# Performance work log

Hardware: AMD Instinct MI355X
Metric: run time of the kernel (lower is better)

## Reference

```python
import jax, jax.numpy as jnp
import numpy as np

N_NODES = 20000
N_EDGES = 320000
IN_CH = 64
OUT_CH = 128

def _gat(x, src, dst, W, a_src, a_dst, bias, concat):
    # PyG GATConv: linear -> per-edge leaky_relu attention logits -> segment softmax over dst -> scatter-weighted sum
    N = x.shape[0]
    H, C = a_src.shape
    xl = (x @ W).reshape(N, H, C)                       # [N,H,C]
    al = (xl * a_src).sum(-1)                           # [N,H] src logits
    ar = (xl * a_dst).sum(-1)                           # [N,H] dst logits
    e = jax.nn.leaky_relu(al[src] + ar[dst], 0.2)       # [E,H]
    emax = jax.ops.segment_max(e, dst, num_segments=N)  # every node has a self loop -> no empty segments
    ee = jnp.exp(e - emax[dst])
    denom = jax.ops.segment_sum(ee, dst, num_segments=N)
    alpha = ee / (denom[dst] + 1e-16)                   # [E,H]
    out = jax.ops.segment_sum(xl[src] * alpha[:, :, None], dst, num_segments=N)  # [N,H,C]
    out = out.reshape(N, H * C) if concat else out.mean(axis=1)
    return out + bias

def setup_inputs() -> dict:
    key = jax.random.key(0)
    ks = jax.random.split(key, 32)
    def lin(k, fi, fo):
        return jax.random.normal(k, (fi, fo), jnp.float32) / np.sqrt(fi)
    def att(k, H, C):
        return jax.random.normal(k, (H, C), jnp.float32) / np.sqrt(C)
    x = jax.random.normal(ks[0], (N_NODES, IN_CH), jnp.float32)
    src = jax.random.randint(ks[1], (N_EDGES,), 0, N_NODES, jnp.int32)
    dst = jax.random.randint(ks[2], (N_EDGES,), 0, N_NODES, jnp.int32)
    dst = jnp.where(dst == src, (dst + 1) % N_NODES, dst)  # avoid pre-existing self loops
    edge_index = jnp.stack([src, dst])
    edge_time = jax.random.uniform(ks[3], (N_EDGES,), jnp.float32)
    H = 4
    return {
        "x": x, "edge_time": edge_time,
        "W1": lin(ks[4], IN_CH, 512), "as1": att(ks[5], H, 128), "ad1": att(ks[6], H, 128), "b1": jnp.zeros((512,), jnp.float32),
        "W2": lin(ks[7], 512, 512),   "as2": att(ks[8], H, 128), "ad2": att(ks[9], H, 128), "b2": jnp.zeros((512,), jnp.float32),
        "W3": lin(ks[10], 512, 512),  "as3": att(ks[11], H, 128), "ad3": att(ks[12], H, 128), "b3": jnp.zeros((OUT_CH,), jnp.float32),
        "tW1": lin(ks[13], 1, 64), "tb1": jnp.zeros((64,), jnp.float32),
        "tW2": lin(ks[14], 64, OUT_CH), "tb2": jnp.zeros((OUT_CH,), jnp.float32),
        "fW1": lin(ks[15], 2 * OUT_CH, OUT_CH), "fb1": jnp.zeros((OUT_CH,), jnp.float32),
        "fW2": lin(ks[16], OUT_CH, OUT_CH), "fb2": jnp.zeros((OUT_CH,), jnp.float32),
        "ln_g": jnp.ones((OUT_CH,), jnp.float32), "ln_b": jnp.zeros((OUT_CH,), jnp.float32),
        "rW": lin(ks[17], IN_CH, OUT_CH), "rb": jnp.zeros((OUT_CH,), jnp.float32),
        "edge_index": edge_index,
    }

def reference(x, edge_time, W1, as1, ad1, b1, W2, as2, ad2, b2, W3, as3, ad3, b3,
              tW1, tb1, tW2, tb2, fW1, fb1, fW2, fb2, ln_g, ln_b, rW, rb, edge_index):
    N = x.shape[0]
    loop = jnp.arange(N, dtype=edge_index.dtype)
    src = jnp.concatenate([edge_index[0], loop])
    dst = jnp.concatenate([edge_index[1], loop])
    # temporal embedding of raw (pre-self-loop) edges
    t = edge_time[:, None]
    time_emb = jax.nn.relu(t @ tW1 + tb1) @ tW2 + tb2    # [E, OUT_CH]
    x_res = x @ rW + rb
    h = jax.nn.relu(_gat(x, src, dst, W1, as1, ad1, b1, True))
    h = jax.nn.relu(_gat(h, src, dst, W2, as2, ad2, b2, True))
    h = jax.nn.relu(_gat(h, src, dst, W3, as3, ad3, b3, False))
    # x_agg[row] += h[col]  with (row, col) = (src, dst) incl. self loops
    agg = jax.ops.segment_sum(h[dst], src, num_segments=N)
    tm = jnp.broadcast_to(time_emb.mean(axis=0)[None, :], (N, time_emb.shape[1]))
    z = jnp.concatenate([agg, tm], axis=1)
    z = jax.nn.relu(z @ fW1 + fb1)                        # dropout is identity in eval
    z = z @ fW2 + fb2
    mu = z.mean(-1, keepdims=True)
    var = ((z - mu) ** 2).mean(-1, keepdims=True)
    z = (z - mu) / jnp.sqrt(var + 1e-5) * ln_g + ln_b
    return z + x_res
```

## Files before the change

### kernel.cpp

```cpp
#include <hip/hip_runtime.h>
#include <hip/hip_bf16.h>
#include <math.h>

typedef short bf16x8 __attribute__((ext_vector_type(8)));
typedef float f32x4 __attribute__((ext_vector_type(4)));

__device__ __forceinline__ float lrelu(float v) { return v > 0.f ? v : 0.2f * v; }

__device__ __forceinline__ void gload16(const void* g, void* l) {
  __builtin_amdgcn_global_load_lds(
      (const __attribute__((address_space(1))) void*)g,
      (__attribute__((address_space(3))) void*)l, 16, 0, 0);
}

__device__ __forceinline__ uint packbf(float v0, float v1) {
  __hip_bfloat16 h0 = __float2bfloat16(v0);
  __hip_bfloat16 h1 = __float2bfloat16(v1);
  return (uint)(*(unsigned short*)&h0) | ((uint)(*(unsigned short*)&h1) << 16);
}

__global__ __launch_bounds__(256) void k_countT(const int* __restrict__ src,
    const int* __restrict__ dst, int E, int* cntD, int* cntS,
    const float* __restrict__ et, const float* __restrict__ tW1,
    const float* __restrict__ tb1, float* __restrict__ tacc) {
  int t = threadIdx.x;
  int e = blockIdx.x * 256 + t;
  if (e < E) {
    atomicAdd(&cntD[dst[e]], 1);
    atomicAdd(&cntS[src[e]], 1);
  }
  if (blockIdx.x < 256) {
    __shared__ float se[256];
    __shared__ float buf[256];
    int l = t & 63, w = t >> 6;
    float wk = tW1[l], bk = tb1[l];
    float a0 = 0.f, a1 = 0.f, a2 = 0.f, a3 = 0.f;
    for (int base = blockIdx.x * 256; base < E; base += 256 * 256) {
      int idx = base + t;
      se[t] = (idx < E) ? et[idx] : 0.f;
      __syncthreads();
      int cnt = E - base; if (cnt > 256) cnt = 256;
      int s0 = w * 64;
      int c = cnt - s0; if (c < 0) c = 0; if (c > 64) c = 64;
      int j = 0;
      for (; j + 4 <= c; j += 4) {
        a0 += fmaxf(se[s0 + j] * wk + bk, 0.f);
        a1 += fmaxf(se[s0 + j + 1] * wk + bk, 0.f);
        a2 += fmaxf(se[s0 + j + 2] * wk + bk, 0.f);
        a3 += fmaxf(se[s0 + j + 3] * wk + bk, 0.f);
      }
      for (; j < c; ++j) a0 += fmaxf(se[s0 + j] * wk + bk, 0.f);
      __syncthreads();
    }
    buf[t] = (a0 + a1) + (a2 + a3);
    __syncthreads();
    if (t < 64) {
      float s = buf[t] + buf[t + 64] + buf[t + 128] + buf[t + 192];
      atomicAdd(&tacc[t], s);
    }
  }
}

__global__ __launch_bounds__(1024) void k_scan2c(const int* __restrict__ cntD, int* __restrict__ offD,
    const int* __restrict__ cntS, int* __restrict__ offS, int n,
    const float* __restrict__ tacc, const float* __restrict__ tW2,
    const float* __restrict__ tb2, const float* __restrict__ fW1,
    const float* __restrict__ fb1, float* __restrict__ cvec, int E) {
  int t = threadIdx.x;
  if (blockIdx.x == 2) {
    __shared__ float tm[128];
    if (t < 128) {
      float inv = 1.f / (float)E;
      float acc = tb2[t];
      for (int k = 0; k < 64; ++k) acc += (tacc[k] * inv) * tW2[k * 128 + t];
      tm[t] = acc;
    }
    __syncthreads();
    if (t < 128) {
      float c = fb1[t];
      for (int k = 0; k < 128; ++k) c += tm[k] * fW1[(128 + k) * 128 + t];
      cvec[t] = c;
    }
    return;
  }
  const int* cnt = blockIdx.x ? cntS : cntD;
  int* off = blockIdx.x ? offS : offD;
  __shared__ int sums[1024];
  int PT = (n + 1023) >> 10;
  int start = t * PT;
  int local = 0;
  for (int i = 0; i < PT; ++i) {
    int idx = start + i;
    if (idx < n) local += cnt[idx];
  }
  sums[t] = local;
  __syncthreads();
  for (int o = 1; o < 1024; o <<= 1) {
    int v = (t >= o) ? sums[t - o] : 0;
    __syncthreads();
    sums[t] += v;
    __syncthreads();
  }
  int run = sums[t] - local;
  for (int i = 0; i < PT; ++i) {
    int idx = start + i;
    if (idx < n) { off[idx] = run; run += cnt[idx]; }
  }
  if (t == 1023) off[n] = run;
}

__global__ void k_fill(const int* __restrict__ src, const int* __restrict__ dst, int E,
                       const int* __restrict__ offD, int* curD, int* lstD,
                       const int* __restrict__ offS, int* curS, int* lstS) {
  int e = blockIdx.x * blockDim.x + threadIdx.x;
  if (e < E) {
    int d = dst[e], s = src[e];
    int p = atomicAdd(&curD[d], 1);
    lstD[offD[d] + p] = s;
    int q = atomicAdd(&curS[s], 1);
    lstS[offS[s] + q] = d;
  }
}

struct PrepArgs {
  const float* W[6]; __hip_bfloat16* Wt[6]; int K[6]; int Nw[6]; int tstart[6];
  int NC, XB;
};

__global__ __launch_bounds__(256) void k_prep(PrepArgs a, const float* __restrict__ x,
    __hip_bfloat16* __restrict__ xbf, __hip_bfloat16* __restrict__ habf,
    __hip_bfloat16* __restrict__ aggbf, int N, int Mp) {
  __shared__ float tile[32][65];
  int bid = blockIdx.x;
  int t = threadIdx.x;
  if (bid < a.NC) {
    int m = 0;
#pragma unroll
    for (int i = 1; i < 6; ++i) if (bid >= a.tstart[i]) m = i;
    const float* W = a.W[m];
    __hip_bfloat16* Wt = a.Wt[m];
    int K = a.K[m], Nw = a.Nw[m];
    int lt = bid - a.tstart[m];
    int ntn = Nw >> 6;
    int bk = (lt / ntn) * 32, bn = (lt % ntn) * 64;
    int rn = t & 63, rk = t >> 6;
#pragma unroll
    for (int i = 0; i < 8; ++i)
      tile[rk + i * 4][rn] = W[(size_t)(bk + rk + i * 4) * Nw + bn + rn];
    __syncthreads();
    int wk2 = (t & 15) * 2, wn = t >> 4;
    uint* Wo = (uint*)Wt;
#pragma unroll
    for (int i = 0; i < 4; ++i) {
      int n = wn + i * 16;
      Wo[((size_t)(bn + n) * K + bk + wk2) >> 1] = packbf(tile[wk2][n], tile[wk2 + 1][n]);
    }
  } else if (bid < a.NC + a.XB) {
    int i4 = (bid - a.NC) * 256 + t;
    int row = i4 >> 4;
    float4 v = make_float4(0.f, 0.f, 0.f, 0.f);
    if (row < N) v = ((const float4*)x)[i4];
    uint2 p; p.x = packbf(v.x, v.y); p.y = packbf(v.z, v.w);
    ((uint2*)xbf)[i4] = p;
  } else {
    int row = N + (bid - a.NC - a.XB);
    ((uint*)habf)[(size_t)row * 256 + t] = 0;
    if (t < 64) ((uint*)aggbf)[(size_t)row * 64 + t] = 0;
  }
}

template<int EPI>
__global__ __launch_bounds__(256) void gemm_t(
    const __hip_bfloat16* __restrict__ A, const __hip_bfloat16* __restrict__ Bt,
    void* __restrict__ Cout, const float* __restrict__ bias,
    int M, int Nw, int K, int relu, int Nn,
    const float* __restrict__ asrc, const float* __restrict__ adst,
    float* __restrict__ al, float* __restrict__ ar,
    float* __restrict__ C2, const float* __restrict__ bias2,
    const float* __restrict__ lng, const float* __restrict__ lnb,
    float* __restrict__ resid)
{
  __shared__ short As0[128 * 32];
  __shared__ short As1[128 * 32];
  __shared__ short Bs0[128 * 32];
  __shared__ short Bs1[128 * 32];
  int tid = threadIdx.x;
  int bm = blockIdx.x * 128;
  int cb = blockIdx.y;
  int bn = cb * 128;
  int w = tid >> 6, l = tid & 63;
  int wr = (w >> 1) * 64, wc = (w & 1) * 64;
  f32x4 acc[4][4] = {};
  const short* Ag = (const short*)A;
  const short* Bg = (const short*)Bt;

  for (int k0 = 0; k0 < K; k0 += 64) {
#pragma unroll
    for (int i = 0; i < 2; ++i) {
      int slot = i * 256 + tid;
      int row = slot >> 2;
      int col = (slot & 3) * 8;
      const short* Arow = Ag + (size_t)(bm + row) * K + k0 + col;
      const short* Brow = Bg + (size_t)(bn + row) * K + k0 + col;
      gload16(Arow, &As0[slot * 8]);
      gload16(Arow + 32, &As1[slot * 8]);
      gload16(Brow, &Bs0[slot * 8]);
      gload16(Brow + 32, &Bs1[slot * 8]);
    }
    __syncthreads();
    {
      bf16x8 af[4], bfr[4];
#pragma unroll
      for (int m = 0; m < 4; ++m)
        af[m] = *(const bf16x8*)&As0[(wr + m * 16 + (l & 15)) * 32 + (l >> 4) * 8];
#pragma unroll
      for (int n = 0; n < 4; ++n)
        bfr[n] = *(const bf16x8*)&Bs0[(wc + n * 16 + (l & 15)) * 32 + (l >> 4) * 8];
#pragma unroll
      for (int m = 0; m < 4; ++m)
#pragma unroll
        for (int n = 0; n < 4; ++n)
          acc[m][n] = __builtin_amdgcn_mfma_f32_16x16x32_bf16(af[m], bfr[n], acc[m][n], 0, 0, 0);
    }
    {
      bf16x8 af[4], bfr[4];
#pragma unroll
      for (int m = 0; m < 4; ++m)
        af[m] = *(const bf16x8*)&As1[(wr + m * 16 + (l & 15)) * 32 + (l >> 4) * 8];
#pragma unroll
      for (int n = 0; n < 4; ++n)
        bfr[n] = *(const bf16x8*)&Bs1[(wc + n * 16 + (l & 15)) * 32 + (l >> 4) * 8];
#pragma unroll
      for (int m = 0; m < 4; ++m)
#pragma unroll
        for (int n = 0; n < 4; ++n)
          acc[m][n] = __builtin_amdgcn_mfma_f32_16x16x32_bf16(af[m], bfr[n], acc[m][n], 0, 0, 0);
    }
    __syncthreads();
  }

  int g = l >> 4, cc = l & 15, cr = g * 4;

  if (EPI == 0) {
#pragma unroll
    for (int n = 0; n < 4; ++n) {
      int col = bn + wc + n * 16 + cc;
      float bb = bias ? bias[col] : 0.f;
#pragma unroll
      for (int m = 0; m < 4; ++m) {
#pragma unroll
        for (int r = 0; r < 4; ++r) {
          int gm = bm + wr + m * 16 + cr + r;
          if (gm < M) {
            float v = acc[m][n][r] + bb;
            if (relu) v = fmaxf(v, 0.f);
            ((__hip_bfloat16*)Cout)[(size_t)gm * Nw + col] = __float2bfloat16(v);
          }
        }
      }
    }
  }

  if (EPI == 1) {
    if (cb < 4) {
#pragma unroll
      for (int n = 0; n < 4; ++n) {
        int col = bn + wc + n * 16 + cc;
#pragma unroll
        for (int m = 0; m < 4; ++m) {
#pragma unroll
          for (int r = 0; r < 4; ++r) {
            int gm = bm + wr + m * 16 + cr + r;
            if (gm < M)
              ((__hip_bfloat16*)Cout)[(size_t)gm * 512 + col] = __float2bfloat16(acc[m][n][r]);
          }
        }
      }
      float asv[4], adv[4];
#pragma unroll
      for (int n = 0; n < 4; ++n) {
        int ch = bn + wc + n * 16 + cc;
        asv[n] = asrc[ch]; adv[n] = adst[ch];
      }
      float* spal = (float*)As0;
      float* spar = spal + 256;
#pragma unroll
      for (int m = 0; m < 4; ++m) {
#pragma unroll
        for (int r = 0; r < 4; ++r) {
          float pa = acc[m][0][r] * asv[0] + acc[m][1][r] * asv[1]
                   + acc[m][2][r] * asv[2] + acc[m][3][r] * asv[3];
          float pb = acc[m][0][r] * adv[0] + acc[m][1][r] * adv[1]
                   + acc[m][2][r] * adv[2] + acc[m][3][r] * adv[3];
#pragma unroll
          for (int o = 1; o < 16; o <<= 1) {
            pa += __shfl_xor(pa, o);
            pb += __shfl_xor(pb, o);
          }
          if (cc == 0) {
            int rl = m * 16 + cr + r;
            spal[w * 64 + rl] = pa;
            spar[w * 64 + rl] = pb;
          }
        }
      }
      __syncthreads();
      if ((w & 1) == 0) {
        float av = spal[w * 64 + l] + spal[(w + 1) * 64 + l];
        float rv = spar[w * 64 + l] + spar[(w + 1) * 64 + l];
        int row = bm + wr + l;
        if (row < Nn) { al[row * 4 + cb] = av; ar[row * 4 + cb] = rv; }
      }
    } else {
#pragma unroll
      for (int n = 0; n < 4; ++n) {
        int col2 = wc + n * 16 + cc;
        float bb = bias2[col2];
#pragma unroll
        for (int m = 0; m < 4; ++m) {
#pragma unroll
          for (int r = 0; r < 4; ++r) {
            int gm = bm + wr + m * 16 + cr + r;
            if (gm < Nn) C2[(size_t)gm * 128 + col2] = acc[m][n][r] + bb;
          }
        }
      }
    }
  }

  if (EPI == 2) {
    float bb[4], gl_[4], gb_[4];
#pragma unroll
    for (int n = 0; n < 4; ++n) {
      int col = wc + n * 16 + cc;
      bb[n] = bias[col]; gl_[n] = lng[col]; gb_[n] = lnb[col];
    }
    float* ssum = (float*)As0;
    float* ssq = ssum + 256;
    float* smu = ssum + 512;
    float* srs = ssum + 640;
#pragma unroll
    for (int m = 0; m < 4; ++m) {
#pragma unroll
      for (int r = 0; r < 4; ++r) {
        float s = 0.f, q = 0.f;
#pragma unroll
        for (int n = 0; n < 4; ++n) {
          float z = acc[m][n][r] + bb[n];
          s += z; q += z * z;
        }
#pragma unroll
        for (int o = 1; o < 16; o <<= 1) {
          s += __shfl_xor(s, o);
          q += __shfl_xor(q, o);
        }
        if (cc == 0) {
          int rl = m * 16 + cr + r;
          ssum[w * 64 + rl] = s;
          ssq[w * 64 + rl] = q;
        }
      }
    }
    __syncthreads();
    if ((w & 1) == 0) {
      float s = ssum[w * 64 + l] + ssum[(w + 1) * 64 + l];
      float q = ssq[w * 64 + l] + ssq[(w + 1) * 64 + l];
      float mu = s * (1.f / 128.f);
      float var = q * (1.f / 128.f) - mu * mu;
      smu[wr + l] = mu;
      srs[wr + l] = rsqrtf(var + 1e-5f);
    }
    __syncthreads();
#pragma unroll
    for (int m = 0; m < 4; ++m) {
#pragma unroll
      for (int r = 0; r < 4; ++r) {
        int rl = wr + m * 16 + cr + r;
        int gm = bm + rl;
        if (gm < M) {
          float mu = smu[rl], rs = srs[rl];
#pragma unroll
          for (int n = 0; n < 4; ++n) {
            int col = wc + n * 16 + cc;
            float z = acc[m][n][r] + bb[n];
            float y = (z - mu) * rs * gl_[n] + gb_[n] + resid[(size_t)gm * 128 + col];
            resid[(size_t)gm * 128 + col] = y;
          }
        }
      }
    }
  }
}

__global__ __launch_bounds__(256) void k_gat_agg(
    const __hip_bfloat16* __restrict__ xl, const float* __restrict__ al,
    const float* __restrict__ ar, const int* __restrict__ off,
    const int* __restrict__ lst, const float* __restrict__ bias,
    __hip_bfloat16* __restrict__ outb, __hip_bfloat16* __restrict__ outh,
    int mode, int N)
{
  __shared__ int   sside[4][64];
  __shared__ float sebuf[4][4][68];
  int w = threadIdx.x >> 6, l = threadIdx.x & 63;
  int d = blockIdx.x * 4 + w;
  bool active = (d < N);
  int base = 0, deg = 0, tot = 0;
  float4 arv = make_float4(0.f, 0.f, 0.f, 0.f);
  if (active) {
    base = off[d]; deg = off[d + 1] - base; tot = deg + 1;
    arv = *(const float4*)(ar + 4 * d);
  }
  int hh = l >> 4;
  float facc[8] = {0.f, 0.f, 0.f, 0.f, 0.f, 0.f, 0.f, 0.f};
  float dn0 = 0.f, dn1 = 0.f, dn2 = 0.f, dn3 = 0.f;
  const uint4* xw = (const uint4*)xl;
  auto fma8 = [&](uint4 pv, float e) {
    facc[0] += e * __uint_as_float(pv.x << 16);
    facc[1] += e * __uint_as_float(pv.x & 0xffff0000u);
    facc[2] += e * __uint_as_float(pv.y << 16);
    facc[3] += e * __uint_as_float(pv.y & 0xffff0000u);
    facc[4] += e * __uint_as_float(pv.z << 16);
    facc[5] += e * __uint_as_float(pv.z & 0xffff0000u);
    facc[6] += e * __uint_as_float(pv.w << 16);
    facc[7] += e * __uint_as_float(pv.w & 0xffff0000u);
  };
  for (int cb = 0; cb < tot; cb += 64) {
    int j = cb + l;
    float e0 = 0.f, e1 = 0.f, e2 = 0.f, e3 = 0.f;
    int sid = 0;
    if (j < tot) {
      sid = (j == deg) ? d : lst[base + j];
      float4 av = *(const float4*)(al + 4 * sid);
      e0 = __expf(lrelu(av.x + arv.x));
      e1 = __expf(lrelu(av.y + arv.y));
      e2 = __expf(lrelu(av.z + arv.z));
      e3 = __expf(lrelu(av.w + arv.w));
      dn0 += e0; dn1 += e1; dn2 += e2; dn3 += e3;
    }
    sside[w][l] = sid;
    sebuf[w][0][l] = e0; sebuf[w][1][l] = e1;
    sebuf[w][2][l] = e2; sebuf[w][3][l] = e3;
    int cnt = tot - cb; if (cnt > 64) cnt = 64;
    int jj = 0;
    for (; jj + 4 <= cnt; jj += 4) {
      int s0 = sside[w][jj], s1 = sside[w][jj + 1];
      int s2 = sside[w][jj + 2], s3 = sside[w][jj + 3];
      float ea = sebuf[w][hh][jj], eb = sebuf[w][hh][jj + 1];
      float ec = sebuf[w][hh][jj + 2], ed = sebuf[w][hh][jj + 3];
      uint4 p0 = xw[(size_t)s0 * 64 + l];
      uint4 p1 = xw[(size_t)s1 * 64 + l];
      uint4 p2 = xw[(size_t)s2 * 64 + l];
      uint4 p3 = xw[(size_t)s3 * 64 + l];
      fma8(p0, ea); fma8(p1, eb); fma8(p2, ec); fma8(p3, ed);
    }
    for (; jj < cnt; ++jj) {
      int s0 = sside[w][jj];
      float ea = sebuf[w][hh][jj];
      uint4 p0 = xw[(size_t)s0 * 64 + l];
      fma8(p0, ea);
    }
  }
#pragma unroll
  for (int o = 1; o < 64; o <<= 1) {
    dn0 += __shfl_xor(dn0, o); dn1 += __shfl_xor(dn1, o);
    dn2 += __shfl_xor(dn2, o); dn3 += __shfl_xor(dn3, o);
  }
  if (!active) return;
  float dsel = hh == 0 ? dn0 : hh == 1 ? dn1 : hh == 2 ? dn2 : dn3;
  float rden = 1.f / dsel;
  if (mode == 0) {
    int c8 = l * 8;
    const float4* bp = (const float4*)(bias + c8);
    float4 b0 = bp[0], b1 = bp[1];
    float vb[8] = {b0.x, b0.y, b0.z, b0.w, b1.x, b1.y, b1.z, b1.w};
    uint4 o4; uint* po = (uint*)&o4;
#pragma unroll
    for (int i = 0; i < 4; ++i) {
      float v0 = fmaxf(facc[2*i]   * rden + vb[2*i],   0.f);
      float v1 = fmaxf(facc[2*i+1] * rden + vb[2*i+1], 0.f);
      po[i] = packbf(v0, v1);
    }
    ((uint4*)outb)[(size_t)d * 64 + l] = o4;
  } else {
#pragma unroll
    for (int i = 0; i < 8; ++i) {
      facc[i] *= rden;
      facc[i] += __shfl_xor(facc[i], 16);
      facc[i] += __shfl_xor(facc[i], 32);
    }
    if (l < 16) {
      int c = l * 8;
      const float4* bp = (const float4*)(bias + c);
      float4 b0 = bp[0], b1 = bp[1];
      float vb[8] = {b0.x, b0.y, b0.z, b0.w, b1.x, b1.y, b1.z, b1.w};
      uint4 o4; uint* po = (uint*)&o4;
#pragma unroll
      for (int i = 0; i < 4; ++i) {
        float v0 = fmaxf(facc[2*i]   * 0.25f + vb[2*i],   0.f);
        float v1 = fmaxf(facc[2*i+1] * 0.25f + vb[2*i+1], 0.f);
        po[i] = packbf(v0, v1);
      }
      ((uint4*)outh)[(size_t)d * 16 + l] = o4;
    }
  }
}

__global__ __launch_bounds__(256) void k_aggsrc(const __hip_bfloat16* __restrict__ h3,
    const int* __restrict__ off, const int* __restrict__ lst,
    __hip_bfloat16* __restrict__ out, int N) {
  int w = threadIdx.x >> 6, l = threadIdx.x & 63;
  int n = blockIdx.x * 4 + w;
  if (n >= N) return;
  const uint* hw = (const uint*)h3;
  uint pv = hw[(size_t)n * 64 + l];
  float a0 = __uint_as_float(pv << 16);
  float a1 = __uint_as_float(pv & 0xffff0000u);
  float b0 = 0.f, b1 = 0.f, c0 = 0.f, c1 = 0.f, d0 = 0.f, d1 = 0.f;
  int b = off[n], e = off[n + 1];
  int j = b;
  for (; j + 4 <= e; j += 4) {
    int s0 = lst[j], s1 = lst[j + 1], s2 = lst[j + 2], s3 = lst[j + 3];
    uint q0 = hw[(size_t)s0 * 64 + l];
    uint q1 = hw[(size_t)s1 * 64 + l];
    uint q2 = hw[(size_t)s2 * 64 + l];
    uint q3 = hw[(size_t)s3 * 64 + l];
    a0 += __uint_as_float(q0 << 16); a1 += __uint_as_float(q0 & 0xffff0000u);
    b0 += __uint_as_float(q1 << 16); b1 += __uint_as_float(q1 & 0xffff0000u);
    c0 += __uint_as_float(q2 << 16); c1 += __uint_as_float(q2 & 0xffff0000u);
    d0 += __uint_as_float(q3 << 16); d1 += __uint_as_float(q3 & 0xffff0000u);
  }
  for (; j < e; ++j) {
    uint q = hw[(size_t)lst[j] * 64 + l];
    a0 += __uint_as_float(q << 16);
    a1 += __uint_as_float(q & 0xffff0000u);
  }
  ((uint*)out)[(size_t)n * 64 + l] = packbf((a0 + b0) + (c0 + d0), (a1 + b1) + (c1 + d1));
}

extern "C" void kernel_launch(void* const* d_in, const int* in_sizes, int n_in,
                              void* d_out, int out_size, void* d_ws, size_t ws_size,
                              hipStream_t stream) {
  (void)n_in; (void)out_size; (void)ws_size;
  const float* x   = (const float*)d_in[0];
  const float* et  = (const float*)d_in[1];
  const float* W1  = (const float*)d_in[2];
  const float* as1 = (const float*)d_in[3];
  const float* ad1 = (const float*)d_in[4];
  const float* b1  = (const float*)d_in[5];
  const float* W2  = (const float*)d_in[6];
  const float* as2 = (const float*)d_in[7];
  const float* ad2 = (const float*)d_in[8];
  const float* b2  = (const float*)d_in[9];
  const float* W3  = (const float*)d_in[10];
  const float* as3 = (const float*)d_in[11];
  const float* ad3 = (const float*)d_in[12];
  const float* b3  = (const float*)d_in[13];
  const float* tW1 = (const float*)d_in[14];
  const float* tb1 = (const float*)d_in[15];
  const float* tW2 = (const float*)d_in[16];
  const float* tb2 = (const float*)d_in[17];
  const float* fW1 = (const float*)d_in[18];
  const float* fb1 = (const float*)d_in[19];
  const float* fW2 = (const float*)d_in[20];
  const float* fb2 = (const float*)d_in[21];
  const float* lng = (const float*)d_in[22];
  const float* lnb = (const float*)d_in[23];
  const float* rW  = (const float*)d_in[24];
  const float* rb  = (const float*)d_in[25];
  const int*   ei  = (const int*)d_in[26];
  const int N = in_sizes[0] / 64;
  const int E = in_sizes[26] / 2;
  const int Mp = ((N + 127) / 128) * 128;
  const int* src = ei;
  const int* dst = ei + E;

  char* cur = (char*)d_ws;
  auto carve = [&](size_t bytes) { char* p = cur; cur += (bytes + 255) & ~(size_t)255; return p; };
  __hip_bfloat16* xbf  = (__hip_bfloat16*)carve((size_t)Mp * 64 * 2);
  __hip_bfloat16* habf = (__hip_bfloat16*)carve((size_t)Mp * 512 * 2);
  __hip_bfloat16* xlbf = (__hip_bfloat16*)carve((size_t)Mp * 512 * 2);
  __hip_bfloat16* wtCat= (__hip_bfloat16*)carve((size_t)640 * 64 * 2);
  __hip_bfloat16* wt2  = (__hip_bfloat16*)carve((size_t)512 * 512 * 2);
  __hip_bfloat16* wt3  = (__hip_bfloat16*)carve((size_t)512 * 512 * 2);
  __hip_bfloat16* wtF1 = (__hip_bfloat16*)carve((size_t)128 * 128 * 2);
  __hip_bfloat16* wtF2 = (__hip_bfloat16*)carve((size_t)128 * 128 * 2);
  __hip_bfloat16* aggbf= (__hip_bfloat16*)carve((size_t)Mp * 128 * 2);
  __hip_bfloat16* z1bf = (__hip_bfloat16*)carve((size_t)Mp * 128 * 2);
  __hip_bfloat16* h3   = (__hip_bfloat16*)carve((size_t)N * 128 * 2);
  float* al   = (float*)carve((size_t)N * 4 * 4);
  float* ar   = (float*)carve((size_t)N * 4 * 4);
  float* cvec = (float*)carve(128 * 4);
  int* offD = (int*)carve((size_t)(N + 1) * 4);
  int* offS = (int*)carve((size_t)(N + 1) * 4);
  int* lstD = (int*)carve((size_t)E * 4);
  int* lstS = (int*)carve((size_t)E * 4);
  char* zstart = cur;
  int* cntD = (int*)carve((size_t)N * 4);
  int* curD = (int*)carve((size_t)N * 4);
  int* cntS = (int*)carve((size_t)N * 4);
  int* curS = (int*)carve((size_t)N * 4);
  float* tacc = (float*)carve(64 * 4);
  size_t zbytes = (size_t)(cur - zstart);
  float* xres = (float*)d_out;

  hipMemsetAsync(zstart, 0, zbytes, stream);

  k_countT<<<(E + 255) / 256, 256, 0, stream>>>(src, dst, E, cntD, cntS, et, tW1, tb1, tacc);
  k_scan2c<<<3, 1024, 0, stream>>>(cntD, offD, cntS, offS, N, tacc, tW2, tb2, fW1, fb1, cvec, E);
  k_fill<<<(E + 255) / 256, 256, 0, stream>>>(src, dst, E, offD, curD, lstD, offS, curS, lstS);

  {
    PrepArgs pa;
    int ts = 0;
    auto setd = [&](int i, const float* W, __hip_bfloat16* Wt, int K, int Nw) {
      pa.W[i] = W; pa.Wt[i] = Wt; pa.K[i] = K; pa.Nw[i] = Nw; pa.tstart[i] = ts;
      ts += (K / 32) * (Nw / 64);
    };
    setd(0, W1, wtCat, 64, 512);
    setd(1, W2, wt2, 512, 512);
    setd(2, W3, wt3, 512, 512);
    setd(3, rW, wtCat + (size_t)512 * 64, 64, 128);
    setd(4, fW1, wtF1, 128, 128);
    setd(5, fW2, wtF2, 128, 128);
    pa.NC = ts;
    pa.XB = Mp / 16;
    int grid = pa.NC + pa.XB + (Mp - N);
    k_prep<<<grid, 256, 0, stream>>>(pa, x, xbf, habf, aggbf, N, Mp);
  }

  const int TB = Mp / 128;
  const int GB = (N + 3) / 4;

  gemm_t<1><<<dim3(TB, 5), 256, 0, stream>>>(xbf, wtCat, xlbf, nullptr, Mp, 640, 64, 0, N,
      as1, ad1, al, ar, xres, rb, nullptr, nullptr, nullptr);
  k_gat_agg<<<GB, 256, 0, stream>>>(xlbf, al, ar, offD, lstD, b1, habf, nullptr, 0, N);
  gemm_t<1><<<dim3(TB, 4), 256, 0, stream>>>(habf, wt2, xlbf, nullptr, Mp, 512, 512, 0, N,
      as2, ad2, al, ar, nullptr, nullptr, nullptr, nullptr, nullptr);
  k_gat_agg<<<GB, 256, 0, stream>>>(xlbf, al, ar, offD, lstD, b2, habf, nullptr, 0, N);
  gemm_t<1><<<dim3(TB, 4), 256, 0, stream>>>(habf, wt3, xlbf, nullptr, Mp, 512, 512, 0, N,
      as3, ad3, al, ar, nullptr, nullptr, nullptr, nullptr, nullptr);
  k_gat_agg<<<GB, 256, 0, stream>>>(xlbf, al, ar, offD, lstD, b3, nullptr, h3, 1, N);

  k_aggsrc<<<GB, 256, 0, stream>>>(h3, offS, lstS, aggbf, N);

  gemm_t<0><<<dim3(TB, 1), 256, 0, stream>>>(aggbf, wtF1, z1bf, cvec, Mp, 128, 128, 1, N,
      nullptr, nullptr, nullptr, nullptr, nullptr, nullptr, nullptr, nullptr, nullptr);
  gemm_t<2><<<dim3(TB, 1), 256, 0, stream>>>(z1bf, wtF2, nullptr, fb2, N, 128, 128, 0, N,
      nullptr, nullptr, nullptr, nullptr, nullptr, nullptr, lng, lnb, xres);
}
```

Baseline: 380.4 us.

## Merge setup kernels, fold CSR fill into first GEMM, fuse FFN GEMMs

Merges the edge-count/time-embedding kernel with the weight-conversion prep kernel into a single launch. Folds the CSR fill pass into extra blocks of the first GEMM grid, so it runs alongside that GEMM. Fuses the two feed-forward GEMMs into one kernel that keeps the intermediate in LDS, removing the z1 round trip through global memory. This cuts launch count and global traffic, at the cost of larger LDS use in the fused FFN kernel and heterogeneous block roles.

```diff
diff --git a/kernel.cpp b/kernel.cpp
--- a/kernel.cpp
+++ b/kernel.cpp
@@ -19,45 +19,94 @@
   return (uint)(*(unsigned short*)&h0) | ((uint)(*(unsigned short*)&h1) << 16);
 }
 
-__global__ __launch_bounds__(256) void k_countT(const int* __restrict__ src,
-    const int* __restrict__ dst, int E, int* cntD, int* cntS,
+struct PrepArgs {
+  const float* W[6]; __hip_bfloat16* Wt[6]; int K[6]; int Nw[6]; int tstart[6];
+  int NC, XB;
+};
+
+__global__ __launch_bounds__(256) void k_build(
+    const int* __restrict__ src, const int* __restrict__ dst, int E,
+    int* cntD, int* cntS,
     const float* __restrict__ et, const float* __restrict__ tW1,
-    const float* __restrict__ tb1, float* __restrict__ tacc) {
+    const float* __restrict__ tb1, float* __restrict__ tacc,
+    PrepArgs a, const float* __restrict__ x,
+    __hip_bfloat16* __restrict__ xbf, __hip_bfloat16* __restrict__ habf,
+    __hip_bfloat16* __restrict__ aggbf, int N, int Mp, int EB) {
+  __shared__ float se[256];
+  __shared__ float buf[256];
+  __shared__ float tile[32][65];
   int t = threadIdx.x;
-  int e = blockIdx.x * 256 + t;
-  if (e < E) {
-    atomicAdd(&cntD[dst[e]], 1);
-    atomicAdd(&cntS[src[e]], 1);
-  }
-  if (blockIdx.x < 256) {
-    __shared__ float se[256];
-    __shared__ float buf[256];
-    int l = t & 63, w = t >> 6;
-    float wk = tW1[l], bk = tb1[l];
-    float a0 = 0.f, a1 = 0.f, a2 = 0.f, a3 = 0.f;
-    for (int base = blockIdx.x * 256; base < E; base += 256 * 256) {
-      int idx = base + t;
-      se[t] = (idx < E) ? et[idx] : 0.f;
+  int bid = blockIdx.x;
+  if (bid < EB) {
+    int e = bid * 256 + t;
+    if (e < E) {
+      atomicAdd(&cntD[dst[e]], 1);
+      atomicAdd(&cntS[src[e]], 1);
+    }
+    if (bid < 256) {
+      int l = t & 63, w = t >> 6;
+      float wk = tW1[l], bk = tb1[l];
+      float a0 = 0.f, a1 = 0.f, a2 = 0.f, a3 = 0.f;
+      for (int base = bid * 256; base < E; base += 256 * 256) {
+        int idx = base + t;
+        se[t] = (idx < E) ? et[idx] : 0.f;
+        __syncthreads();
+        int cnt = E - base; if (cnt > 256) cnt = 256;
+        int s0 = w * 64;
+        int c = cnt - s0; if (c < 0) c = 0; if (c > 64) c = 64;
+        int j = 0;
+        for (; j + 4 <= c; j += 4) {
+          a0 += fmaxf(se[s0 + j] * wk + bk, 0.f);
+          a1 += fmaxf(se[s0 + j + 1] * wk + bk, 0.f);
+          a2 += fmaxf(se[s0 + j + 2] * wk + bk, 0.f);
+          a3 += fmaxf(se[s0 + j + 3] * wk + bk, 0.f);
+        }
+        for (; j < c; ++j) a0 += fmaxf(se[s0 + j] * wk + bk, 0.f);
+        __syncthreads();
+      }
+      buf[t] = (a0 + a1) + (a2 + a3);
       __syncthreads();
-      int cnt = E - base; if (cnt > 256) cnt = 256;
-      int s0 = w * 64;
-      int c = cnt - s0; if (c < 0) c = 0; if (c > 64) c = 64;
-      int j = 0;
-      for (; j + 4 <= c; j += 4) {
-        a0 += fmaxf(se[s0 + j] * wk + bk, 0.f);
-        a1 += fmaxf(se[s0 + j + 1] * wk + bk, 0.f);
-        a2 += fmaxf(se[s0 + j + 2] * wk + bk, 0.f);
-        a3 += fmaxf(se[s0 + j + 3] * wk + bk, 0.f);
-      }
-      for (; j < c; ++j) a0 += fmaxf(se[s0 + j] * wk + bk, 0.f);
-      __syncthreads();
-    }
-    buf[t] = (a0 + a1) + (a2 + a3);
-    __syncthreads();
-    if (t < 64) {
-      float s = buf[t] + buf[t + 64] + buf[t + 128] + buf[t + 192];
-      atomicAdd(&tacc[t], s);
-    }
+      if (t < 64) {
+        float s = buf[t] + buf[t + 64] + buf[t + 128] + buf[t + 192];
+        atomicAdd(&tacc[t], s);
+      }
+    }
+    return;
+  }
+  int pbid = bid - EB;
+  if (pbid < a.NC) {
+    int m = 0;
+#pragma unroll
+    for (int i = 1; i < 6; ++i) if (pbid >= a.tstart[i]) m = i;
+    const float* W = a.W[m];
+    __hip_bfloat16* Wt = a.Wt[m];
+    int K = a.K[m], Nw = a.Nw[m];
+    int lt = pbid - a.tstart[m];
+    int ntn = Nw >> 6;
+    int bk = (lt / ntn) * 32, bn = (lt % ntn) * 64;
+    int rn = t & 63, rk = t >> 6;
+#pragma unroll
+    for (int i = 0; i < 8; ++i)
+      tile[rk + i * 4][rn] = W[(size_t)(bk + rk + i * 4) * Nw + bn + rn];
+    __syncthreads();
+    int wk2 = (t & 15) * 2, wn = t >> 4;
+    uint* Wo = (uint*)Wt;
+#pragma unroll
+    for (int i = 0; i < 4; ++i) {
+      int n = wn + i * 16;
+      Wo[((size_t)(bn + n) * K + bk + wk2) >> 1] = packbf(tile[wk2][n], tile[wk2 + 1][n]);
+    }
+  } else if (pbid < a.NC + a.XB) {
+    int i4 = (pbid - a.NC) * 256 + t;
+    int row = i4 >> 4;
+    float4 v = make_float4(0.f, 0.f, 0.f, 0.f);
+    if (row < N) v = ((const float4*)x)[i4];
+    uint2 p; p.x = packbf(v.x, v.y); p.y = packbf(v.z, v.w);
+    ((uint2*)xbf)[i4] = p;
+  } else {
+    int row = N + (pbid - a.NC - a.XB);
+    ((uint*)habf)[(size_t)row * 256 + t] = 0;
+    if (t < 64) ((uint*)aggbf)[(size_t)row * 64 + t] = 0;
   }
 }
 
@@ -109,81 +158,34 @@
   if (t == 1023) off[n] = run;
 }
 
-__global__ void k_fill(const int* __restrict__ src, const int* __restrict__ dst, int E,
-                       const int* __restrict__ offD, int* curD, int* lstD,
-                       const int* __restrict__ offS, int* curS, int* lstS) {
-  int e = blockIdx.x * blockDim.x + threadIdx.x;
-  if (e < E) {
-    int d = dst[e], s = src[e];
-    int p = atomicAdd(&curD[d], 1);
-    lstD[offD[d] + p] = s;
-    int q = atomicAdd(&curS[s], 1);
-    lstS[offS[s] + q] = d;
-  }
-}
-
-struct PrepArgs {
-  const float* W[6]; __hip_bfloat16* Wt[6]; int K[6]; int Nw[6]; int tstart[6];
-  int NC, XB;
-};
-
-__global__ __launch_bounds__(256) void k_prep(PrepArgs a, const float* __restrict__ x,
-    __hip_bfloat16* __restrict__ xbf, __hip_bfloat16* __restrict__ habf,
-    __hip_bfloat16* __restrict__ aggbf, int N, int Mp) {
-  __shared__ float tile[32][65];
-  int bid = blockIdx.x;
-  int t = threadIdx.x;
-  if (bid < a.NC) {
-    int m = 0;
-#pragma unroll
-    for (int i = 1; i < 6; ++i) if (bid >= a.tstart[i]) m = i;
-    const float* W = a.W[m];
-    __hip_bfloat16* Wt = a.Wt[m];
-    int K = a.K[m], Nw = a.Nw[m];
-    int lt = bid - a.tstart[m];
-    int ntn = Nw >> 6;
-    int bk = (lt / ntn) * 32, bn = (lt % ntn) * 64;
-    int rn = t & 63, rk = t >> 6;
-#pragma unroll
-    for (int i = 0; i < 8; ++i)
-      tile[rk + i * 4][rn] = W[(size_t)(bk + rk + i * 4) * Nw + bn + rn];
-    __syncthreads();
-    int wk2 = (t & 15) * 2, wn = t >> 4;
-    uint* Wo = (uint*)Wt;
-#pragma unroll
-    for (int i = 0; i < 4; ++i) {
-      int n = wn + i * 16;
-      Wo[((size_t)(bn + n) * K + bk + wk2) >> 1] = packbf(tile[wk2][n], tile[wk2 + 1][n]);
-    }
-  } else if (bid < a.NC + a.XB) {
-    int i4 = (bid - a.NC) * 256 + t;
-    int row = i4 >> 4;
-    float4 v = make_float4(0.f, 0.f, 0.f, 0.f);
-    if (row < N) v = ((const float4*)x)[i4];
-    uint2 p; p.x = packbf(v.x, v.y); p.y = packbf(v.z, v.w);
-    ((uint2*)xbf)[i4] = p;
-  } else {
-    int row = N + (bid - a.NC - a.XB);
-    ((uint*)habf)[(size_t)row * 256 + t] = 0;
-    if (t < 64) ((uint*)aggbf)[(size_t)row * 64 + t] = 0;
-  }
-}
-
-template<int EPI>
-__global__ __launch_bounds__(256) void gemm_t(
+__global__ __launch_bounds__(256) void gemm_e1(
     const __hip_bfloat16* __restrict__ A, const __hip_bfloat16* __restrict__ Bt,
-    void* __restrict__ Cout, const float* __restrict__ bias,
-    int M, int Nw, int K, int relu, int Nn,
+    void* __restrict__ Cout, int M, int Nn, int K,
     const float* __restrict__ asrc, const float* __restrict__ adst,
     float* __restrict__ al, float* __restrict__ ar,
     float* __restrict__ C2, const float* __restrict__ bias2,
-    const float* __restrict__ lng, const float* __restrict__ lnb,
-    float* __restrict__ resid)
+    int TBx,
+    const int* __restrict__ fsrc, const int* __restrict__ fdst, int fE,
+    const int* __restrict__ foffD, int* fcurD, int* flstD,
+    const int* __restrict__ foffS, int* fcurS, int* flstS)
 {
   __shared__ short As0[128 * 32];
   __shared__ short As1[128 * 32];
   __shared__ short Bs0[128 * 32];
   __shared__ short Bs1[128 * 32];
+  if ((int)blockIdx.x >= TBx) {
+    if (blockIdx.y == 0) {
+      int e = ((int)blockIdx.x - TBx) * 256 + (int)threadIdx.x;
+      if (e < fE) {
+        int d = fdst[e], s = fsrc[e];
+        int p = atomicAdd(&fcurD[d], 1);
+        flstD[foffD[d] + p] = s;
+        int q = atomicAdd(&fcurS[s], 1);
+        flstS[foffS[s] + q] = d;
+      }
+    }
+    return;
+  }
   int tid = threadIdx.x;
   int bm = blockIdx.x * 128;
   int cb = blockIdx.y;
@@ -241,151 +243,259 @@
 
   int g = l >> 4, cc = l & 15, cr = g * 4;
 
-  if (EPI == 0) {
+  if (cb < 4) {
 #pragma unroll
     for (int n = 0; n < 4; ++n) {
       int col = bn + wc + n * 16 + cc;
-      float bb = bias ? bias[col] : 0.f;
 #pragma unroll
       for (int m = 0; m < 4; ++m) {
 #pragma unroll
         for (int r = 0; r < 4; ++r) {
           int gm = bm + wr + m * 16 + cr + r;
-          if (gm < M) {
-            float v = acc[m][n][r] + bb;
-            if (relu) v = fmaxf(v, 0.f);
-            ((__hip_bfloat16*)Cout)[(size_t)gm * Nw + col] = __float2bfloat16(v);
-          }
+          if (gm < M)
+            ((__hip_bfloat16*)Cout)[(size_t)gm * 512 + col] = __float2bfloat16(acc[m][n][r]);
         }
       }
     }
-  }
-
-  if (EPI == 1) {
-    if (cb < 4) {
-#pragma unroll
-      for (int n = 0; n < 4; ++n) {
-        int col = bn + wc + n * 16 + cc;
-#pragma unroll
-        for (int m = 0; m < 4; ++m) {
-#pragma unroll
-          for (int r = 0; r < 4; ++r) {
-            int gm = bm + wr + m * 16 + cr + r;
-            if (gm < M)
-              ((__hip_bfloat16*)Cout)[(size_t)gm * 512 + col] = __float2bfloat16(acc[m][n][r]);
-          }
-        }
-      }
-      float asv[4], adv[4];
-#pragma unroll
-      for (int n = 0; n < 4; ++n) {
-        int ch = bn + wc + n * 16 + cc;
-        asv[n] = asrc[ch]; adv[n] = adst[ch];
-      }
-      float* spal = (float*)As0;
-      float* spar = spal + 256;
-#pragma unroll
-      for (int m = 0; m < 4; ++m) {
-#pragma unroll
-        for (int r = 0; r < 4; ++r) {
-          float pa = acc[m][0][r] * asv[0] + acc[m][1][r] * asv[1]
-                   + acc[m][2][r] * asv[2] + acc[m][3][r] * asv[3];
-          float pb = acc[m][0][r] * adv[0] + acc[m][1][r] * adv[1]
-                   + acc[m][2][r] * adv[2] + acc[m][3][r] * adv[3];
-#pragma unroll
-          for (int o = 1; o < 16; o <<= 1) {
-            pa += __shfl_xor(pa, o);
-            pb += __shfl_xor(pb, o);
-          }
-          if (cc == 0) {
-            int rl = m * 16 + cr + r;
-            spal[w * 64 + rl] = pa;
-            spar[w * 64 + rl] = pb;
-          }
-        }
-      }
-      __syncthreads();
-      if ((w & 1) == 0) {
-        float av = spal[w * 64 + l] + spal[(w + 1) * 64 + l];
-        float rv = spar[w * 64 + l] + spar[(w + 1) * 64 + l];
-        int row = bm + wr + l;
-        if (row < Nn) { al[row * 4 + cb] = av; ar[row * 4 + cb] = rv; }
-      }
-    } else {
-#pragma unroll
-      for (int n = 0; n < 4; ++n) {
-        int col2 = wc + n * 16 + cc;
-        float bb = bias2[col2];
-#pragma unroll
-        for (int m = 0; m < 4; ++m) {
-#pragma unroll
-          for (int r = 0; r < 4; ++r) {
-            int gm = bm + wr + m * 16 + cr + r;
-            if (gm < Nn) C2[(size_t)gm * 128 + col2] = acc[m][n][r] + bb;
-          }
-        }
-      }
-    }
-  }
-
-  if (EPI == 2) {
-    float bb[4], gl_[4], gb_[4];
+    float asv[4], adv[4];
 #pragma unroll
     for (int n = 0; n < 4; ++n) {
-      int col = wc + n * 16 + cc;
-      bb[n] = bias[col]; gl_[n] = lng[col]; gb_[n] = lnb[col];
-    }
-    float* ssum = (float*)As0;
-    float* ssq = ssum + 256;
-    float* smu = ssum + 512;
-    float* srs = ssum + 640;
+      int ch = bn + wc + n * 16 + cc;
+      asv[n] = asrc[ch]; adv[n] = adst[ch];
+    }
+    float* spal = (float*)As0;
+    float* spar = spal + 256;
 #pragma unroll
     for (int m = 0; m < 4; ++m) {
 #pragma unroll
       for (int r = 0; r < 4; ++r) {
-        float s = 0.f, q = 0.f;
-#pragma unroll
-        for (int n = 0; n < 4; ++n) {
-          float z = acc[m][n][r] + bb[n];
-          s += z; q += z * z;
-        }
+        float pa = acc[m][0][r] * asv[0] + acc[m][1][r] * asv[1]
+                 + acc[m][2][r] * asv[2] + acc[m][3][r] * asv[3];
+        float pb = acc[m][0][r] * adv[0] + acc[m][1][r] * adv[1]
+                 + acc[m][2][r] * adv[2] + acc[m][3][r] * adv[3];
 #pragma unroll
         for (int o = 1; o < 16; o <<= 1) {
-          s += __shfl_xor(s, o);
-          q += __shfl_xor(q, o);
+          pa += __shfl_xor(pa, o);
+          pb += __shfl_xor(pb, o);
         }
         if (cc == 0) {
           int rl = m * 16 + cr + r;
-          ssum[w * 64 + rl] = s;
-          ssq[w * 64 + rl] = q;
+          spal[w * 64 + rl] = pa;
+          spar[w * 64 + rl] = pb;
         }
       }
     }
     __syncthreads();
     if ((w & 1) == 0) {
-      float s = ssum[w * 64 + l] + ssum[(w + 1) * 64 + l];
-      float q = ssq[w * 64 + l] + ssq[(w + 1) * 64 + l];
-      float mu = s * (1.f / 128.f);
-      float var = q * (1.f / 128.f) - mu * mu;
-      smu[wr + l] = mu;
-      srs[wr + l] = rsqrtf(var + 1e-5f);
-    }
-    __syncthreads();
+      float av = spal[w * 64 + l] + spal[(w + 1) * 64 + l];
+      float rv = spar[w * 64 + l] + spar[(w + 1) * 64 + l];
+      int row = bm + wr + l;
+      if (row < Nn) { al[row * 4 + cb] = av; ar[row * 4 + cb] = rv; }
+    }
+  } else {
+#pragma unroll
+    for (int n = 0; n < 4; ++n) {
+      int col2 = wc + n * 16 + cc;
+      float bb = bias2[col2];
+#pragma unroll
+      for (int m = 0; m < 4; ++m) {
+#pragma unroll
+        for (int r = 0; r < 4; ++r) {
+          int gm = bm + wr + m * 16 + cr + r;
+          if (gm < Nn) C2[(size_t)gm * 128 + col2] = acc[m][n][r] + bb;
+        }
+      }
+    }
+  }
+}
+
+__global__ __launch_bounds__(256) void gemm_ff(
+    const __hip_bfloat16* __restrict__ A, const __hip_bfloat16* __restrict__ B1t,
+    const __hip_bfloat16* __restrict__ B2t, const float* __restrict__ cvec,
+    const float* __restrict__ fb2, const float* __restrict__ lng,
+    const float* __restrict__ lnb, float* __restrict__ resid, int M)
+{
+  __shared__ char ldsraw[32768 + 128 * 136 * 2];
+  short* As0 = (short*)ldsraw;
+  short* As1 = As0 + 4096;
+  short* Bs0 = As1 + 4096;
+  short* Bs1 = Bs0 + 4096;
+  short* z1s = (short*)(ldsraw + 32768);
+  int tid = threadIdx.x;
+  int bm = blockIdx.x * 128;
+  int w = tid >> 6, l = tid & 63;
+  int wr = (w >> 1) * 64, wc = (w & 1) * 64;
+  int g = l >> 4, cc = l & 15, cr = g * 4;
+  const short* Ag = (const short*)A;
+  const short* B1 = (const short*)B1t;
+  const short* B2 = (const short*)B2t;
+  f32x4 acc[4][4] = {};
+
+  for (int k0 = 0; k0 < 128; k0 += 64) {
+#pragma unroll
+    for (int i = 0; i < 2; ++i) {
+      int slot = i * 256 + tid;
+      int row = slot >> 2;
+      int col = (slot & 3) * 8;
+      const short* Arow = Ag + (size_t)(bm + row) * 128 + k0 + col;
+      const short* Brow = B1 + (size_t)row * 128 + k0 + col;
+      gload16(Arow, &As0[slot * 8]);
+      gload16(Arow + 32, &As1[slot * 8]);
+      gload16(Brow, &Bs0[slot * 8]);
+      gload16(Brow + 32, &Bs1[slot * 8]);
+    }
+    __syncthreads();
+    {
+      bf16x8 af[4], bfr[4];
+#pragma unroll
+      for (int m = 0; m < 4; ++m)
+        af[m] = *(const bf16x8*)&As0[(wr + m * 16 + (l & 15)) * 32 + (l >> 4) * 8];
+#pragma unroll
+      for (int n = 0; n < 4; ++n)
+        bfr[n] = *(const bf16x8*)&Bs0[(wc + n * 16 + (l & 15)) * 32 + (l >> 4) * 8];
+#pragma unroll
+      for (int m = 0; m < 4; ++m)
+#pragma unroll
+        for (int n = 0; n < 4; ++n)
+          acc[m][n] = __builtin_amdgcn_mfma_f32_16x16x32_bf16(af[m], bfr[n], acc[m][n], 0, 0, 0);
+    }
+    {
+      bf16x8 af[4], bfr[4];
+#pragma unroll
+      for (int m = 0; m < 4; ++m)
+        af[m] = *(const bf16x8*)&As1[(wr + m * 16 + (l & 15)) * 32 + (l >> 4) * 8];
+#pragma unroll
+      for (int n = 0; n < 4; ++n)
+        bfr[n] = *(const bf16x8*)&Bs1[(wc + n * 16 + (l & 15)) * 32 + (l >> 4) * 8];
+#pragma unroll
+      for (int m = 0; m < 4; ++m)
+#pragma unroll
+        for (int n = 0; n < 4; ++n)
+          acc[m][n] = __builtin_amdgcn_mfma_f32_16x16x32_bf16(af[m], bfr[n], acc[m][n], 0, 0, 0);
+    }
+    __syncthreads();
+  }
+
+#pragma unroll
+  for (int n = 0; n < 4; ++n) {
+    int col = wc + n * 16 + cc;
+    float bb = cvec[col];
 #pragma unroll
     for (int m = 0; m < 4; ++m) {
 #pragma unroll
       for (int r = 0; r < 4; ++r) {
         int rl = wr + m * 16 + cr + r;
-        int gm = bm + rl;
-        if (gm < M) {
-          float mu = smu[rl], rs = srs[rl];
-#pragma unroll
-          for (int n = 0; n < 4; ++n) {
-            int col = wc + n * 16 + cc;
-            float z = acc[m][n][r] + bb[n];
-            float y = (z - mu) * rs * gl_[n] + gb_[n] + resid[(size_t)gm * 128 + col];
-            resid[(size_t)gm * 128 + col] = y;
-          }
+        float v = fmaxf(acc[m][n][r] + bb, 0.f);
+        __hip_bfloat16 hb = __float2bfloat16(v);
+        z1s[rl * 136 + col] = *(short*)&hb;
+      }
+    }
+  }
+#pragma unroll
+  for (int m = 0; m < 4; ++m)
+#pragma unroll
+    for (int n = 0; n < 4; ++n)
+      acc[m][n] = (f32x4){0.f, 0.f, 0.f, 0.f};
+  __syncthreads();
+
+  for (int k0 = 0; k0 < 128; k0 += 64) {
+#pragma unroll
+    for (int i = 0; i < 2; ++i) {
+      int slot = i * 256 + tid;
+      int row = slot >> 2;
+      int col = (slot & 3) * 8;
+      const short* Brow = B2 + (size_t)row * 128 + k0 + col;
+      gload16(Brow, &Bs0[slot * 8]);
+      gload16(Brow + 32, &Bs1[slot * 8]);
+    }
+    __syncthreads();
+    {
+      bf16x8 af[4], bfr[4];
+#pragma unroll
+      for (int m = 0; m < 4; ++m)
+        af[m] = *(const bf16x8*)&z1s[(wr + m * 16 + (l & 15)) * 136 + k0 + (l >> 4) * 8];
+#pragma unroll
+      for (int n = 0; n < 4; ++n)
+        bfr[n] = *(const bf16x8*)&Bs0[(wc + n * 16 + (l & 15)) * 32 + (l >> 4) * 8];
+#pragma unroll
+      for (int m = 0; m < 4; ++m)
+#pragma unroll
+        for (int n = 0; n < 4; ++n)
+          acc[m][n] = __builtin_amdgcn_mfma_f32_16x16x32_bf16(af[m], bfr[n], acc[m][n], 0, 0, 0);
+    }
+    {
+      bf16x8 af[4], bfr[4];
+#pragma unroll
+      for (int m = 0; m < 4; ++m)
+        af[m] = *(const bf16x8*)&z1s[(wr + m * 16 + (l & 15)) * 136 + k0 + 32 + (l >> 4) * 8];
+#pragma unroll
+      for (int n = 0; n < 4; ++n)
+        bfr[n] = *(const bf16x8*)&Bs1[(wc + n * 16 + (l & 15)) * 32 + (l >> 4) * 8];
+#pragma unroll
+      for (int m = 0; m < 4; ++m)
+#pragma unroll
+        for (int n = 0; n < 4; ++n)
+          acc[m][n] = __builtin_amdgcn_mfma_f32_16x16x32_bf16(af[m], bfr[n], acc[m][n], 0, 0, 0);
+    }
+    __syncthreads();
+  }
+
+  float bb[4], gl_[4], gb_[4];
+#pragma unroll
+  for (int n = 0; n < 4; ++n) {
+    int col = wc + n * 16 + cc;
+    bb[n] = fb2[col]; gl_[n] = lng[col]; gb_[n] = lnb[col];
+  }
+  float* ssum = (float*)As0;
+  float* ssq = ssum + 256;
+  float* smu = ssum + 512;
+  float* srs = ssum + 640;
+#pragma unroll
+  for (int m = 0; m < 4; ++m) {
+#pragma unroll
+    for (int r = 0; r < 4; ++r) {
+      float s = 0.f, q = 0.f;
+#pragma unroll
+      for (int n = 0; n < 4; ++n) {
+        float z = acc[m][n][r] + bb[n];
+        s += z; q += z * z;
+      }
+#pragma unroll
+      for (int o = 1; o < 16; o <<= 1) {
+        s += __shfl_xor(s, o);
+        q += __shfl_xor(q, o);
+      }
+      if (cc == 0) {
+        int rl = m * 16 + cr + r;
+        ssum[w * 64 + rl] = s;
+        ssq[w * 64 + rl] = q;
+      }
+    }
+  }
+  __syncthreads();
+  if ((w & 1) == 0) {
+    float s = ssum[w * 64 + l] + ssum[(w + 1) * 64 + l];
+    float q = ssq[w * 64 + l] + ssq[(w + 1) * 64 + l];
+    float mu = s * (1.f / 128.f);
+    float var = q * (1.f / 128.f) - mu * mu;
+    smu[wr + l] = mu;
+    srs[wr + l] = rsqrtf(var + 1e-5f);
+  }
+  __syncthreads();
+#pragma unroll
+  for (int m = 0; m < 4; ++m) {
+#pragma unroll
+    for (int r = 0; r < 4; ++r) {
+      int rl = wr + m * 16 + cr + r;
+      int gm = bm + rl;
+      if (gm < M) {
+        float mu = smu[rl], rs = srs[rl];
+#pragma unroll
+        for (int n = 0; n < 4; ++n) {
+          int col = wc + n * 16 + cc;
+          float z = acc[m][n][r] + bb[n];
+          float y = (z - mu) * rs * gl_[n] + gb_[n] + resid[(size_t)gm * 128 + col];
+          resid[(size_t)gm * 128 + col] = y;
         }
       }
     }
@@ -585,7 +695,6 @@
   __hip_bfloat16* wtF1 = (__hip_bfloat16*)carve((size_t)128 * 128 * 2);
   __hip_bfloat16* wtF2 = (__hip_bfloat16*)carve((size_t)128 * 128 * 2);
   __hip_bfloat16* aggbf= (__hip_bfloat16*)carve((size_t)Mp * 128 * 2);
-  __hip_bfloat16* z1bf = (__hip_bfloat16*)carve((size_t)Mp * 128 * 2);
   __hip_bfloat16* h3   = (__hip_bfloat16*)carve((size_t)N * 128 * 2);
   float* al   = (float*)carve((size_t)N * 4 * 4);
   float* ar   = (float*)carve((size_t)N * 4 * 4);
@@ -605,12 +714,9 @@
 
   hipMemsetAsync(zstart, 0, zbytes, stream);
 
-  k_countT<<<(E + 255) / 256, 256, 0, stream>>>(src, dst, E, cntD, cntS, et, tW1, tb1, tacc);
-  k_scan2c<<<3, 1024, 0, stream>>>(cntD, offD, cntS, offS, N, tacc, tW2, tb2, fW1, fb1, cvec, E);
-  k_fill<<<(E + 255) / 256, 256, 0, stream>>>(src, dst, E, offD, curD, lstD, offS, curS, lstS);
-
+  const int EB = (E + 255) / 256;
+  PrepArgs pa;
   {
-    PrepArgs pa;
     int ts = 0;
     auto setd = [&](int i, const float* W, __hip_bfloat16* Wt, int K, int Nw) {
       pa.W[i] = W; pa.Wt[i] = Wt; pa.K[i] = K; pa.Nw[i] = Nw; pa.tstart[i] = ts;
@@ -624,27 +730,30 @@
     setd(5, fW2, wtF2, 128, 128);
     pa.NC = ts;
     pa.XB = Mp / 16;
-    int grid = pa.NC + pa.XB + (Mp - N);
-    k_prep<<<grid, 256, 0, stream>>>(pa, x, xbf, habf, aggbf, N, Mp);
-  }
+    int grid = EB + pa.NC + pa.XB + (Mp - N);
+    k_build<<<grid, 256, 0, stream>>>(src, dst, E, cntD, cntS, et, tW1, tb1, tacc,
+                                      pa, x, xbf, habf, aggbf, N, Mp, EB);
+  }
+  k_scan2c<<<3, 1024, 0, stream>>>(cntD, offD, cntS, offS, N, tacc, tW2, tb2, fW1, fb1, cvec, E);
 
   const int TB = Mp / 128;
   const int GB = (N + 3) / 4;
-
-  gemm_t<1><<<dim3(TB, 5), 256, 0, stream>>>(xbf, wtCat, xlbf, nullptr, Mp, 640, 64, 0, N,
-      as1, ad1, al, ar, xres, rb, nullptr, nullptr, nullptr);
+  const int BIG = 1 << 30;
+
+  gemm_e1<<<dim3(TB + EB, 5), 256, 0, stream>>>(xbf, wtCat, xlbf, Mp, N, 64,
+      as1, ad1, al, ar, xres, rb,
+      TB, src, dst, E, offD, curD, lstD, offS, curS, lstS);
   k_gat_agg<<<GB, 256, 0, stream>>>(xlbf, al, ar, offD, lstD, b1, habf, nullptr, 0, N);
-  gemm_t<1><<<dim3(TB, 4), 256, 0, stream>>>(habf, wt2, xlbf, nullptr, Mp, 512, 512, 0, N,
-      as2, ad2, al, ar, nullptr, nullptr, nullptr, nullptr, nullptr);
+  gemm_e1<<<dim3(TB, 4), 256, 0, stream>>>(habf, wt2, xlbf, Mp, N, 512,
+      as2, ad2, al, ar, nullptr, nullptr,
+      BIG, nullptr, nullptr, 0, nullptr, nullptr, nullptr, nullptr, nullptr, nullptr);
   k_gat_agg<<<GB, 256, 0, stream>>>(xlbf, al, ar, offD, lstD, b2, habf, nullptr, 0, N);
-  gemm_t<1><<<dim3(TB, 4), 256, 0, stream>>>(habf, wt3, xlbf, nullptr, Mp, 512, 512, 0, N,
-      as3, ad3, al, ar, nullptr, nullptr, nullptr, nullptr, nullptr);
+  gemm_e1<<<dim3(TB, 4), 256, 0, stream>>>(habf, wt3, xlbf, Mp, N, 512,
+      as3, ad3, al, ar, nullptr, nullptr,
+      BIG, nullptr, nullptr, 0, nullptr, nullptr, nullptr, nullptr, nullptr, nullptr);
   k_gat_agg<<<GB, 256, 0, stream>>>(xlbf, al, ar, offD, lstD, b3, nullptr, h3, 1, N);
 
   k_aggsrc<<<GB, 256, 0, stream>>>(h3, offS, lstS, aggbf, N);
 
-  gemm_t<0><<<dim3(TB, 1), 256, 0, stream>>>(aggbf, wtF1, z1bf, cvec, Mp, 128, 128, 1, N,
-      nullptr, nullptr, nullptr, nullptr, nullptr, nullptr, nullptr, nullptr, nullptr);
-  gemm_t<2><<<dim3(TB, 1), 256, 0, stream>>>(z1bf, wtF2, nullptr, fb2, N, 128, 128, 0, N,
-      nullptr, nullptr, nullptr, nullptr, nullptr, nullptr, lng, lnb, xres);
-}
+  gemm_ff<<<TB, 256, 0, stream>>>(aggbf, wtF1, wtF2, cvec, fb2, lng, lnb, xres, N);
+}
```

Result: faster. 368.0 us (-3.3%).
